# Optimization experiments

Hardware: AMD Instinct MI355X
Metric: run time of the kernel (lower is better)

## Reference

```python
import jax, jax.numpy as jnp
import numpy as np

H = 16       # query heads
KV = 4       # kv heads
BASE = 10000.0


def _rope(seq_len, head_dim, dtype):
    inv_freq = 1.0 / (BASE ** (jnp.arange(0, head_dim, 2, dtype=jnp.float32) / head_dim))
    t = jnp.arange(seq_len, dtype=jnp.float32)
    freqs = jnp.einsum('i,j->ij', t, inv_freq)          # [S, D/2]
    emb = jnp.concatenate([freqs, freqs], axis=-1)      # [S, D]
    return jnp.cos(emb).astype(dtype), jnp.sin(emb).astype(dtype)


def _rotate_half(x):
    x1, x2 = jnp.split(x, 2, axis=-1)
    return jnp.concatenate([-x2, x1], axis=-1)


def setup_inputs() -> dict:
    key = jax.random.key(0)
    ks = jax.random.split(key, 5)
    B, S, E = 2, 2048, 1024
    return {
        'x': jax.random.normal(ks[0], (B, S, E), jnp.float32),
        'wq': jax.random.normal(ks[1], (E, E), jnp.float32) * (E ** -0.5),
        'wk': jax.random.normal(ks[2], (KV * (E // H), E), jnp.float32) * (E ** -0.5),
        'wv': jax.random.normal(ks[3], (KV * (E // H), E), jnp.float32) * (E ** -0.5),
        'wo': jax.random.normal(ks[4], (E, E), jnp.float32) * (E ** -0.5),
    }


def reference(x, wq, wk, wv, wo):
    B, S, E = x.shape
    D = E // H
    G = H // KV  # query heads per kv head
    scale = D ** -0.5

    q = (x @ wq.T).reshape(B, S, H, D).transpose(0, 2, 1, 3)    # [B,H,S,D]
    k = (x @ wk.T).reshape(B, S, KV, D).transpose(0, 2, 1, 3)   # [B,KV,S,D]
    v = (x @ wv.T).reshape(B, S, KV, D).transpose(0, 2, 1, 3)   # [B,KV,S,D]

    cos, sin = _rope(S, D, x.dtype)                              # [S,D] each
    q = q * cos + _rotate_half(q) * sin
    k = k * cos + _rotate_half(k) * sin

    # GQA: group query heads per kv head instead of materializing repeated K/V
    qg = q.reshape(B, KV, G, S, D)
    scores = jnp.einsum('bkgsd,bktd->bkgst', qg, k) * scale      # [B,KV,G,S,S]
    causal = jnp.triu(jnp.ones((S, S), dtype=bool), k=1)
    scores = jnp.where(causal, jnp.finfo(scores.dtype).min, scores)
    attn = jax.nn.softmax(scores, axis=-1)
    out = jnp.einsum('bkgst,bktd->bkgsd', attn, v)               # [B,KV,G,S,D]
    out = out.reshape(B, H, S, D).transpose(0, 2, 1, 3).reshape(B, S, E)
    return out @ wo.T
```

## Files before the change

kernel.cpp:

```cpp
#include <hip/hip_runtime.h>
#include <stdint.h>

typedef unsigned short u16;
typedef __attribute__((ext_vector_type(8))) short s16x8;
typedef __attribute__((ext_vector_type(4))) float f32x4;
typedef __attribute__((ext_vector_type(4))) unsigned short u16x4;
typedef __attribute__((ext_vector_type(2))) unsigned int u32x2;


__device__ __forceinline__ u16 f2bf(float f) {
  unsigned u = __float_as_uint(f);
  unsigned r = (u + 0x7fffu + ((u >> 16) & 1u)) >> 16;
  return (u16)r;
}
__device__ __forceinline__ unsigned cvt_pk(float lo, float hi) {
  unsigned r;
  asm("v_cvt_pk_bf16_f32 %0, %1, %2" : "=v"(r) : "v"(lo), "v"(hi));
  return r;
}
__device__ __forceinline__ float exp2fast(float x) {
  return __builtin_amdgcn_exp2f(x);
}

typedef const __attribute__((address_space(1))) unsigned int* gas_ptr;
typedef __attribute__((address_space(3))) unsigned int* las_ptr;

__device__ __forceinline__ void g2l16(const void* g, void* l) {
  __builtin_amdgcn_global_load_lds((gas_ptr)g, (las_ptr)l, 16, 0, 0);
}

__device__ __forceinline__ void cvt4(const float* __restrict__ in, u16* __restrict__ out) {
  const f32x4 v = *(const f32x4*)in;
  u16x4 o;
  o[0] = f2bf(v[0]); o[1] = f2bf(v[1]); o[2] = f2bf(v[2]); o[3] = f2bf(v[3]);
  *(u16x4*)out = o;
}


__global__ void prep_kernel(const float* __restrict__ x,  const float* __restrict__ wq,
                            const float* __restrict__ wk, const float* __restrict__ wv,
                            const float* __restrict__ wo,
                            u16* __restrict__ xb, u16* __restrict__ wcat, u16* __restrict__ wob,
                            float* __restrict__ cosT, float* __restrict__ sinT) {
  const long id = (long)blockIdx.x * 256 + threadIdx.x;
  if (id < 262144) {
    cvt4(wq + id * 4, wcat + id * 4);
  } else if (id < 327680) {
    const long i = id - 262144;
    cvt4(wk + i * 4, wcat + 1048576 + i * 4);
  } else if (id < 393216) {
    const long i = id - 327680;
    cvt4(wv + i * 4, wcat + 1310720 + i * 4);
  } else if (id < 655360) {
    const long i = id - 393216;
    cvt4(wo + i * 4, wob + i * 4);
  } else if (id < 671744) {
    const long t = id - 655360;
#pragma unroll
    for (int u = 0; u < 4; ++u) {
      const long idx = t * 4 + u;
      const int s = (int)(idx >> 5), j = (int)(idx & 31);
      const double invd = exp(-(double)j * 0.2878231366242558);
      const float a = (float)s * (float)invd;
      cosT[idx] = cosf(a);
      sinT[idx] = sinf(a);
    }
  } else {
    const long i = id - 671744;
    cvt4(x + i * 4, xb + i * 4);
  }
}


__global__ __launch_bounds__(256, 2) void gemm_qkv_kernel(
    const u16* __restrict__ A, const u16* __restrict__ W,
    u16* __restrict__ qo, u16* __restrict__ ko, u16* __restrict__ vto,
    const float* __restrict__ cosT, const float* __restrict__ sinT) {
  const int K = 1024;
  __shared__ __align__(16) u16 As[2][128 * 64];
  __shared__ __align__(16) u16 Bs[2][128 * 64];
  const int tid = threadIdx.x;
  const int lane = tid & 63;
  const int wave = tid >> 6;
  const int g = lane >> 4, l15 = lane & 15;
  const int wr = wave >> 1, wc = wave & 1;
  const int bid = blockIdx.x;
  const int arowBlk = (bid & 7) * 4 + ((bid >> 3) & 3);
  const int wcolBlk = bid >> 5;
  const long arow0 = (long)arowBlk * 128;
  const long wrow0 = (long)wcolBlk * 128;
  const u16* Ab = A + arow0 * K;
  const u16* Wb = W + wrow0 * K;
  const bool isV = (wcolBlk >= 10);

  auto STAGE = [&](int buf, int k0) {
#pragma unroll
    for (int i = 0; i < 4; ++i) {
      const int lbase = i * 256 + wave * 64;
      const int c = lbase + lane;
      const int r = c >> 3, c8 = c & 7;
      const int cs = (c8 ^ (r & 7)) * 8;
      g2l16(Ab + (long)r * K + k0 + cs, (char*)As[buf] + lbase * 16);
      g2l16(Wb + (long)r * K + k0 + cs, (char*)Bs[buf] + lbase * 16);
    }
  };

  f32x4 acc[4][4] = {};
  int cur = 0;
  STAGE(0, 0);

  for (int k0 = 0; k0 < K; k0 += 64) {
    if (k0 + 64 < K) {
      STAGE(cur ^ 1, k0 + 64);
      asm volatile("s_waitcnt vmcnt(8)" ::: "memory");
    } else {
      asm volatile("s_waitcnt vmcnt(0)" ::: "memory");
    }
    __builtin_amdgcn_s_barrier();
#pragma unroll
    for (int ks = 0; ks < 2; ++ks) {
      s16x8 af[4], bfr[4];
#pragma unroll
      for (int m = 0; m < 4; ++m) {
        const int row = wr * 64 + m * 16 + l15;
        af[m] = *(const s16x8*)((const char*)As[cur] + row * 128 + (((ks * 4 + g) ^ (row & 7)) << 4));
      }
#pragma unroll
      for (int n = 0; n < 4; ++n) {
        const int row = wc * 64 + n * 16 + l15;
        bfr[n] = *(const s16x8*)((const char*)Bs[cur] + row * 128 + (((ks * 4 + g) ^ (row & 7)) << 4));
      }
      __builtin_amdgcn_s_setprio(1);
      if (!isV) {
#pragma unroll
        for (int m = 0; m < 4; ++m)
#pragma unroll
          for (int n = 0; n < 4; ++n)
            acc[m][n] = __builtin_amdgcn_mfma_f32_16x16x32_bf16(af[m], bfr[n], acc[m][n], 0, 0, 0);
      } else {
#pragma unroll
        for (int m = 0; m < 4; ++m)
#pragma unroll
          for (int n = 0; n < 4; ++n)
            acc[m][n] = __builtin_amdgcn_mfma_f32_16x16x32_bf16(bfr[m], af[n], acc[m][n], 0, 0, 0);
      }
      __builtin_amdgcn_s_setprio(0);
    }
    __builtin_amdgcn_s_barrier();
    cur ^= 1;
  }

  const int colBase = (int)wrow0 + wc * 64;
  const int j0 = l15;
  const float QSCALE = 0.18033688011112042f;

  if (colBase < 1024) {
    const int h2 = colBase >> 6;
#pragma unroll
    for (int m = 0; m < 4; ++m) {
      const int grow = (int)arow0 + wr * 64 + m * 16 + g * 4;
#pragma unroll
      for (int r = 0; r < 4; ++r) {
        const int row = grow + r;
        const int s = row & 2047, bb = row >> 11;
        const long ob = (((long)(bb * 16 + h2)) * 2048 + s) * 64;
        const float c0 = cosT[s * 32 + j0],      s0 = sinT[s * 32 + j0];
        const float c1 = cosT[s * 32 + 16 + j0], s1 = sinT[s * 32 + 16 + j0];
        qo[ob + j0]      = f2bf((acc[m][0][r] * c0 - acc[m][2][r] * s0) * QSCALE);
        qo[ob + 16 + j0] = f2bf((acc[m][1][r] * c1 - acc[m][3][r] * s1) * QSCALE);
        qo[ob + 32 + j0] = f2bf((acc[m][2][r] * c0 + acc[m][0][r] * s0) * QSCALE);
        qo[ob + 48 + j0] = f2bf((acc[m][3][r] * c1 + acc[m][1][r] * s1) * QSCALE);
      }
    }
  } else if (colBase < 1280) {
    const int kvh2 = (colBase - 1024) >> 6;
#pragma unroll
    for (int m = 0; m < 4; ++m) {
      const int grow = (int)arow0 + wr * 64 + m * 16 + g * 4;
#pragma unroll
      for (int r = 0; r < 4; ++r) {
        const int row = grow + r;
        const int s = row & 2047, bb = row >> 11;
        const long ob = (((long)(bb * 4 + kvh2)) * 2048 + s) * 64;
        const float c0 = cosT[s * 32 + j0],      s0 = sinT[s * 32 + j0];
        const float c1 = cosT[s * 32 + 16 + j0], s1 = sinT[s * 32 + 16 + j0];
        ko[ob + j0]      = f2bf(acc[m][0][r] * c0 - acc[m][2][r] * s0);
        ko[ob + 16 + j0] = f2bf(acc[m][1][r] * c1 - acc[m][3][r] * s1);
        ko[ob + 32 + j0] = f2bf(acc[m][2][r] * c0 + acc[m][0][r] * s0);
        ko[ob + 48 + j0] = f2bf(acc[m][3][r] * c1 + acc[m][1][r] * s1);
      }
    }
  } else {
    const int kvh2 = (colBase - 1280) >> 6;
    const int bb = (int)(arow0 >> 11);
    const int sBase = (int)(arow0 & 2047) + wr * 64;
    const long vrow0 = ((long)(bb * 4 + kvh2)) * 64;
#pragma unroll
    for (int mw = 0; mw < 4; ++mw) {
      const int d0 = mw * 16 + g * 4;
#pragma unroll
      for (int r = 0; r < 4; ++r) {
        const long db = (vrow0 + d0 + r) * 2048;
#pragma unroll
        for (int nx = 0; nx < 4; ++nx)
          vto[db + sBase + nx * 16 + l15] = f2bf(acc[mw][nx][r]);
      }
    }
  }
}


__global__ __launch_bounds__(256, 2) void gemm_out_kernel(
    const u16* __restrict__ A, const u16* __restrict__ W, float* __restrict__ Y) {
  const int K = 1024, N = 1024;
  __shared__ __align__(16) u16 As[2][128 * 64];
  __shared__ __align__(16) u16 Bs[2][128 * 64];
  const int tid = threadIdx.x;
  const int lane = tid & 63;
  const int wave = tid >> 6;
  const int g = lane >> 4, l15 = lane & 15;
  const int wr = wave >> 1, wc = wave & 1;
  const int bid = blockIdx.x;
  const int arowBlk = (bid & 7) * 4 + ((bid >> 3) & 3);
  const int wcolBlk = bid >> 5;
  const long arow0 = (long)arowBlk * 128;
  const long wrow0 = (long)wcolBlk * 128;
  const u16* Ab = A + arow0 * K;
  const u16* Wb = W + wrow0 * K;

  auto STAGE = [&](int buf, int k0) {
#pragma unroll
    for (int i = 0; i < 4; ++i) {
      const int lbase = i * 256 + wave * 64;
      const int c = lbase + lane;
      const int r = c >> 3, c8 = c & 7;
      const int cs = (c8 ^ (r & 7)) * 8;
      g2l16(Ab + (long)r * K + k0 + cs, (char*)As[buf] + lbase * 16);
      g2l16(Wb + (long)r * K + k0 + cs, (char*)Bs[buf] + lbase * 16);
    }
  };

  f32x4 acc[4][4] = {};
  int cur = 0;
  STAGE(0, 0);

  for (int k0 = 0; k0 < K; k0 += 64) {
    if (k0 + 64 < K) {
      STAGE(cur ^ 1, k0 + 64);
      asm volatile("s_waitcnt vmcnt(8)" ::: "memory");
    } else {
      asm volatile("s_waitcnt vmcnt(0)" ::: "memory");
    }
    __builtin_amdgcn_s_barrier();
#pragma unroll
    for (int ks = 0; ks < 2; ++ks) {
      s16x8 af[4], bfr[4];
#pragma unroll
      for (int m = 0; m < 4; ++m) {
        const int row = wr * 64 + m * 16 + l15;
        af[m] = *(const s16x8*)((const char*)As[cur] + row * 128 + (((ks * 4 + g) ^ (row & 7)) << 4));
      }
#pragma unroll
      for (int n = 0; n < 4; ++n) {
        const int row = wc * 64 + n * 16 + l15;
        bfr[n] = *(const s16x8*)((const char*)Bs[cur] + row * 128 + (((ks * 4 + g) ^ (row & 7)) << 4));
      }
      __builtin_amdgcn_s_setprio(1);
#pragma unroll
      for (int m = 0; m < 4; ++m)
#pragma unroll
        for (int n = 0; n < 4; ++n)
          acc[m][n] = __builtin_amdgcn_mfma_f32_16x16x32_bf16(af[m], bfr[n], acc[m][n], 0, 0, 0);
      __builtin_amdgcn_s_setprio(0);
    }
    __builtin_amdgcn_s_barrier();
    cur ^= 1;
  }

#pragma unroll
  for (int m = 0; m < 4; ++m)
#pragma unroll
    for (int n = 0; n < 4; ++n) {
      const long gr0 = arow0 + wr * 64 + m * 16 + g * 4;
      const long gc = wrow0 + wc * 64 + n * 16 + l15;
#pragma unroll
      for (int r = 0; r < 4; ++r)
        Y[(gr0 + r) * N + gc] = acc[m][n][r];
    }
}


__global__ __launch_bounds__(256, 3) void flash_kernel(
    const u16* __restrict__ qg,
    const u16* __restrict__ kg,
    const u16* __restrict__ vtg,
    u16* __restrict__ og) {
  const int tid = threadIdx.x, lane = tid & 63, w = tid >> 6;
  const int g = lane >> 4, l15 = lane & 15;

  const int bid = blockIdx.x;
  const int lid = (bid & 7) * 128 + (bid >> 3);
  const int qtIdx = lid & 31;
  const int h = (lid >> 5) & 15;
  const int b = lid >> 9;
  const int qt = (qtIdx & 1) ? (31 - (qtIdx >> 1)) : (qtIdx >> 1);
  const int kvh = h >> 2;

  __shared__ __align__(16) u16 Kl[2][64 * 64];
  __shared__ __align__(16) u16 Vl[2][64 * 64];
  __shared__ __align__(16) u16 Pl[4][16][72];

  const u16* Kp = kg  + ((long)(b * 4 + kvh)) * 2048 * 64;
  const u16* Vp = vtg + ((long)(b * 4 + kvh)) * 64 * 2048;

  auto STAGE = [&](int buf, int kt) {
#pragma unroll
    for (int j = 0; j < 2; ++j) {
      const int lbase = j * 256 + w * 64;
      const int c = lbase + lane;
      const int row = c >> 3, c8 = c & 7;
      const int cs = (c8 ^ (row & 7)) * 8;
      g2l16(Kp + ((long)(kt * 64 + row)) * 64 + cs, (char*)Kl[buf] + lbase * 16);
      g2l16(Vp + (long)row * 2048 + kt * 64 + cs,  (char*)Vl[buf] + lbase * 16);
    }
  };

  const u16* Qp = qg + (((long)(b * 16 + h)) * 2048 + qt * 64 + w * 16) * 64;
  const s16x8 qf0 = *(const s16x8*)(Qp + l15 * 64 + g * 8);
  const s16x8 qf1 = *(const s16x8*)(Qp + l15 * 64 + 32 + g * 8);

  f32x4 of[4] = {};
  float m = -1e30f, lsum = 0.f;
  const int qrow = qt * 64 + w * 16 + l15;

  int cur = 0;
  STAGE(0, 0);

#pragma unroll 1
  for (int kt = 0; kt <= qt; ++kt) {
    if (kt < qt) {
      STAGE(cur ^ 1, kt + 1);
      asm volatile("s_waitcnt vmcnt(4)" ::: "memory");
    } else {
      asm volatile("s_waitcnt vmcnt(0)" ::: "memory");
    }
    __builtin_amdgcn_s_barrier();
    const u16* Kb = Kl[cur];
    const u16* Vb = Vl[cur];

    f32x4 sf[4] = {};
    __builtin_amdgcn_s_setprio(1);
#pragma unroll
    for (int ks = 0; ks < 2; ++ks) {
      const s16x8 qv = ks ? qf1 : qf0;
#pragma unroll
      for (int fn = 0; fn < 4; ++fn) {
        const int row = fn * 16 + l15;
        const s16x8 kf = *(const s16x8*)((const char*)Kb + row * 128 + (((ks * 4 + g) ^ (row & 7)) << 4));
        sf[fn] = __builtin_amdgcn_mfma_f32_16x16x32_bf16(kf, qv, sf[fn], 0, 0, 0);
      }
    }
    __builtin_amdgcn_s_setprio(0);

    const bool diag = (kt == qt);
    float p[16];
#pragma unroll
    for (int fn = 0; fn < 4; ++fn)
#pragma unroll
      for (int r = 0; r < 4; ++r) {
        float sv = sf[fn][r];
        if (diag) {
          const int kv = kt * 64 + fn * 16 + 4 * g + r;
          if (kv > qrow) sv = -1e30f;
        }
        p[fn * 4 + r] = sv;
      }
    const float t0 = fmaxf(fmaxf(p[0], p[1]), p[2]);
    const float t1 = fmaxf(fmaxf(p[3], p[4]), p[5]);
    const float t2 = fmaxf(fmaxf(p[6], p[7]), p[8]);
    const float t3 = fmaxf(fmaxf(p[9], p[10]), p[11]);
    const float t4 = fmaxf(fmaxf(p[12], p[13]), p[14]);
    float mx = fmaxf(fmaxf(fmaxf(t0, t1), t2), fmaxf(fmaxf(t3, t4), p[15]));
    mx = fmaxf(mx, __shfl_xor(mx, 16));
    mx = fmaxf(mx, __shfl_xor(mx, 32));

    if (!__all(mx - m <= 11.0f)) {
      const float mn = fmaxf(m, mx);
      const float al = exp2fast(m - mn);
      m = mn;
      lsum *= al;
      float alq[4];
#pragma unroll
      for (int r = 0; r < 4; ++r) alq[r] = __shfl(al, 4 * g + r);
#pragma unroll
      for (int fd = 0; fd < 4; ++fd)
#pragma unroll
        for (int r = 0; r < 4; ++r) of[fd][r] *= alq[r];
    }

#pragma unroll
    for (int i = 0; i < 16; ++i) p[i] = exp2fast(p[i] - m);
    const float s0 = (p[0] + p[1]) + (p[2] + p[3]);
    const float s1 = (p[4] + p[5]) + (p[6] + p[7]);
    const float s2 = (p[8] + p[9]) + (p[10] + p[11]);
    const float s3 = (p[12] + p[13]) + (p[14] + p[15]);
    float rs = (s0 + s1) + (s2 + s3);
    rs += __shfl_xor(rs, 16);
    rs += __shfl_xor(rs, 32);
    lsum += rs;

    u16* Pw = &Pl[w][l15][0];
#pragma unroll
    for (int fn = 0; fn < 4; ++fn) {
      const u32x2 v2 = {cvt_pk(p[fn * 4 + 0], p[fn * 4 + 1]),
                        cvt_pk(p[fn * 4 + 2], p[fn * 4 + 3])};
      *(u32x2*)(Pw + fn * 16 + g * 4) = v2;
    }

    __builtin_amdgcn_s_setprio(1);
#pragma unroll
    for (int ks = 0; ks < 2; ++ks) {
      const s16x8 pa = *(const s16x8*)(&Pl[w][l15][ks * 32 + g * 8]);
#pragma unroll
      for (int fd = 0; fd < 4; ++fd) {
        const int vrow = fd * 16 + l15;
        const s16x8 vf = *(const s16x8*)((const char*)Vb + vrow * 128 + (((ks * 4 + g) ^ (vrow & 7)) << 4));
        of[fd] = __builtin_amdgcn_mfma_f32_16x16x32_bf16(pa, vf, of[fd], 0, 0, 0);
      }
    }
    __builtin_amdgcn_s_setprio(0);

    __builtin_amdgcn_s_barrier();
    cur ^= 1;
  }

  float linv[4];
#pragma unroll
  for (int r = 0; r < 4; ++r) linv[r] = 1.0f / __shfl(lsum, 4 * g + r);
  const long orow0 = (long)b * 2048 + qt * 64 + w * 16 + 4 * g;
#pragma unroll
  for (int r = 0; r < 4; ++r) {
    const long gb = (orow0 + r) * 1024 + h * 64;
#pragma unroll
    for (int fd = 0; fd < 4; ++fd)
      og[gb + fd * 16 + l15] = f2bf(of[fd][r] * linv[r]);
  }
}


extern "C" void kernel_launch(void* const* d_in, const int* in_sizes, int n_in,
                              void* d_out, int out_size, void* d_ws, size_t ws_size,
                              hipStream_t stream) {
  (void)in_sizes; (void)n_in; (void)out_size; (void)ws_size;
  const float* x  = (const float*)d_in[0];
  const float* wq = (const float*)d_in[1];
  const float* wk = (const float*)d_in[2];
  const float* wv = (const float*)d_in[3];
  const float* wo = (const float*)d_in[4];
  float* out = (float*)d_out;

  char* p = (char*)d_ws;
  auto alloc = [&](size_t bytes) { char* r = p; p += (bytes + 255) & ~(size_t)255; return r; };

  u16* xb    = (u16*)alloc(4096ull * 1024 * 2);
  u16* wcat  = (u16*)alloc(1536ull * 1024 * 2);
  u16* wob   = (u16*)alloc(1024ull * 1024 * 2);
  u16* qrb   = (u16*)alloc(4096ull * 1024 * 2);
  u16* krb   = (u16*)alloc(4096ull * 256 * 2);
  u16* vtb   = (u16*)alloc(4096ull * 256 * 2);
  u16* aob   = (u16*)alloc(4096ull * 1024 * 2);
  float* cosT = (float*)alloc(2048ull * 32 * 4);
  float* sinT = (float*)alloc(2048ull * 32 * 4);

  prep_kernel<<<6720, 256, 0, stream>>>(x, wq, wk, wv, wo, xb, wcat, wob, cosT, sinT);

  gemm_qkv_kernel<<<384, 256, 0, stream>>>(xb, wcat, qrb, krb, vtb, cosT, sinT);

  flash_kernel<<<1024, 256, 0, stream>>>(qrb, krb, vtb, aob);

  gemm_out_kernel<<<256, 256, 0, stream>>>(aob, wob, out);
}
```

Measured before the change: 194.0 us.

## Deepen GEMM pipelines to four stages and restructure flash attention tiling

Both GEMM kernels switch from a double-buffered K=64 pipeline to a four-deep K=32 pipeline with a new LDS swizzle. This keeps more global loads in flight and hides memory latency. The flash kernel now processes 128-key tiles, and each block handles a pair of query tiles (qt and 31-qt) in two passes, which balances the causal workload and halves the grid. The price is more LDS per flash block, occupancy reduced to 2, and extra P staging through LDS.

Measured after the change: 187.2 us. 1.04x faster.

```diff
diff --git a/kernel.cpp b/kernel.cpp
--- a/kernel.cpp
+++ b/kernel.cpp
@@ -77,8 +77,8 @@
     u16* __restrict__ qo, u16* __restrict__ ko, u16* __restrict__ vto,
     const float* __restrict__ cosT, const float* __restrict__ sinT) {
   const int K = 1024;
-  __shared__ __align__(16) u16 As[2][128 * 64];
-  __shared__ __align__(16) u16 Bs[2][128 * 64];
+  __shared__ __align__(16) u16 As[4][128 * 32];
+  __shared__ __align__(16) u16 Bs[4][128 * 32];
   const int tid = threadIdx.x;
   const int lane = tid & 63;
   const int wave = tid >> 6;
@@ -95,59 +95,61 @@
 
   auto STAGE = [&](int buf, int k0) {
 #pragma unroll
-    for (int i = 0; i < 4; ++i) {
-      const int lbase = i * 256 + wave * 64;
+    for (int j = 0; j < 2; ++j) {
+      const int lbase = j * 256 + wave * 64;
       const int c = lbase + lane;
-      const int r = c >> 3, c8 = c & 7;
-      const int cs = (c8 ^ (r & 7)) * 8;
+      const int r = c >> 2, c4 = c & 3;
+      const int cs = (c4 ^ ((r >> 1) & 3)) * 8;
       g2l16(Ab + (long)r * K + k0 + cs, (char*)As[buf] + lbase * 16);
       g2l16(Wb + (long)r * K + k0 + cs, (char*)Bs[buf] + lbase * 16);
     }
   };
 
   f32x4 acc[4][4] = {};
-  int cur = 0;
-  STAGE(0, 0);
-
-  for (int k0 = 0; k0 < K; k0 += 64) {
-    if (k0 + 64 < K) {
-      STAGE(cur ^ 1, k0 + 64);
+  STAGE(0, 0); STAGE(1, 32); STAGE(2, 64);
+
+#pragma unroll 1
+  for (int t = 0; t < 32; ++t) {
+    if (t < 29) {
+      STAGE((t + 3) & 3, (t + 3) * 32);
+      asm volatile("s_waitcnt vmcnt(12)" ::: "memory");
+    } else if (t == 29) {
       asm volatile("s_waitcnt vmcnt(8)" ::: "memory");
+    } else if (t == 30) {
+      asm volatile("s_waitcnt vmcnt(4)" ::: "memory");
     } else {
       asm volatile("s_waitcnt vmcnt(0)" ::: "memory");
     }
     __builtin_amdgcn_s_barrier();
-#pragma unroll
-    for (int ks = 0; ks < 2; ++ks) {
-      s16x8 af[4], bfr[4];
-#pragma unroll
-      for (int m = 0; m < 4; ++m) {
-        const int row = wr * 64 + m * 16 + l15;
-        af[m] = *(const s16x8*)((const char*)As[cur] + row * 128 + (((ks * 4 + g) ^ (row & 7)) << 4));
-      }
-#pragma unroll
-      for (int n = 0; n < 4; ++n) {
-        const int row = wc * 64 + n * 16 + l15;
-        bfr[n] = *(const s16x8*)((const char*)Bs[cur] + row * 128 + (((ks * 4 + g) ^ (row & 7)) << 4));
-      }
-      __builtin_amdgcn_s_setprio(1);
-      if (!isV) {
-#pragma unroll
-        for (int m = 0; m < 4; ++m)
-#pragma unroll
-          for (int n = 0; n < 4; ++n)
-            acc[m][n] = __builtin_amdgcn_mfma_f32_16x16x32_bf16(af[m], bfr[n], acc[m][n], 0, 0, 0);
-      } else {
-#pragma unroll
-        for (int m = 0; m < 4; ++m)
-#pragma unroll
-          for (int n = 0; n < 4; ++n)
-            acc[m][n] = __builtin_amdgcn_mfma_f32_16x16x32_bf16(bfr[m], af[n], acc[m][n], 0, 0, 0);
-      }
-      __builtin_amdgcn_s_setprio(0);
-    }
+    const u16* Ac = As[t & 3];
+    const u16* Bc = Bs[t & 3];
+    s16x8 af[4], bfr[4];
+#pragma unroll
+    for (int m = 0; m < 4; ++m) {
+      const int row = wr * 64 + m * 16 + l15;
+      af[m] = *(const s16x8*)((const char*)Ac + row * 64 + ((g ^ ((row >> 1) & 3)) << 4));
+    }
+#pragma unroll
+    for (int n = 0; n < 4; ++n) {
+      const int row = wc * 64 + n * 16 + l15;
+      bfr[n] = *(const s16x8*)((const char*)Bc + row * 64 + ((g ^ ((row >> 1) & 3)) << 4));
+    }
+    __builtin_amdgcn_s_setprio(1);
+    if (!isV) {
+#pragma unroll
+      for (int m = 0; m < 4; ++m)
+#pragma unroll
+        for (int n = 0; n < 4; ++n)
+          acc[m][n] = __builtin_amdgcn_mfma_f32_16x16x32_bf16(af[m], bfr[n], acc[m][n], 0, 0, 0);
+    } else {
+#pragma unroll
+      for (int m = 0; m < 4; ++m)
+#pragma unroll
+        for (int n = 0; n < 4; ++n)
+          acc[m][n] = __builtin_amdgcn_mfma_f32_16x16x32_bf16(bfr[m], af[n], acc[m][n], 0, 0, 0);
+    }
+    __builtin_amdgcn_s_setprio(0);
     __builtin_amdgcn_s_barrier();
-    cur ^= 1;
   }
 
   const int colBase = (int)wrow0 + wc * 64;
@@ -213,8 +215,8 @@
 __global__ __launch_bounds__(256, 2) void gemm_out_kernel(
     const u16* __restrict__ A, const u16* __restrict__ W, float* __restrict__ Y) {
   const int K = 1024, N = 1024;
-  __shared__ __align__(16) u16 As[2][128 * 64];
-  __shared__ __align__(16) u16 Bs[2][128 * 64];
+  __shared__ __align__(16) u16 As[4][128 * 32];
+  __shared__ __align__(16) u16 Bs[4][128 * 32];
   const int tid = threadIdx.x;
   const int lane = tid & 63;
   const int wave = tid >> 6;
@@ -230,51 +232,53 @@
 
   auto STAGE = [&](int buf, int k0) {
 #pragma unroll
-    for (int i = 0; i < 4; ++i) {
-      const int lbase = i * 256 + wave * 64;
+    for (int j = 0; j < 2; ++j) {
+      const int lbase = j * 256 + wave * 64;
       const int c = lbase + lane;
-      const int r = c >> 3, c8 = c & 7;
-      const int cs = (c8 ^ (r & 7)) * 8;
+      const int r = c >> 2, c4 = c & 3;
+      const int cs = (c4 ^ ((r >> 1) & 3)) * 8;
       g2l16(Ab + (long)r * K + k0 + cs, (char*)As[buf] + lbase * 16);
       g2l16(Wb + (long)r * K + k0 + cs, (char*)Bs[buf] + lbase * 16);
     }
   };
 
   f32x4 acc[4][4] = {};
-  int cur = 0;
-  STAGE(0, 0);
-
-  for (int k0 = 0; k0 < K; k0 += 64) {
-    if (k0 + 64 < K) {
-      STAGE(cur ^ 1, k0 + 64);
+  STAGE(0, 0); STAGE(1, 32); STAGE(2, 64);
+
+#pragma unroll 1
+  for (int t = 0; t < 32; ++t) {
+    if (t < 29) {
+      STAGE((t + 3) & 3, (t + 3) * 32);
+      asm volatile("s_waitcnt vmcnt(12)" ::: "memory");
+    } else if (t == 29) {
       asm volatile("s_waitcnt vmcnt(8)" ::: "memory");
+    } else if (t == 30) {
+      asm volatile("s_waitcnt vmcnt(4)" ::: "memory");
     } else {
       asm volatile("s_waitcnt vmcnt(0)" ::: "memory");
     }
     __builtin_amdgcn_s_barrier();
-#pragma unroll
-    for (int ks = 0; ks < 2; ++ks) {
-      s16x8 af[4], bfr[4];
-#pragma unroll
-      for (int m = 0; m < 4; ++m) {
-        const int row = wr * 64 + m * 16 + l15;
-        af[m] = *(const s16x8*)((const char*)As[cur] + row * 128 + (((ks * 4 + g) ^ (row & 7)) << 4));
-      }
-#pragma unroll
-      for (int n = 0; n < 4; ++n) {
-        const int row = wc * 64 + n * 16 + l15;
-        bfr[n] = *(const s16x8*)((const char*)Bs[cur] + row * 128 + (((ks * 4 + g) ^ (row & 7)) << 4));
-      }
-      __builtin_amdgcn_s_setprio(1);
-#pragma unroll
-      for (int m = 0; m < 4; ++m)
-#pragma unroll
-        for (int n = 0; n < 4; ++n)
-          acc[m][n] = __builtin_amdgcn_mfma_f32_16x16x32_bf16(af[m], bfr[n], acc[m][n], 0, 0, 0);
-      __builtin_amdgcn_s_setprio(0);
-    }
+    const u16* Ac = As[t & 3];
+    const u16* Bc = Bs[t & 3];
+    s16x8 af[4], bfr[4];
+#pragma unroll
+    for (int m = 0; m < 4; ++m) {
+      const int row = wr * 64 + m * 16 + l15;
+      af[m] = *(const s16x8*)((const char*)Ac + row * 64 + ((g ^ ((row >> 1) & 3)) << 4));
+    }
+#pragma unroll
+    for (int n = 0; n < 4; ++n) {
+      const int row = wc * 64 + n * 16 + l15;
+      bfr[n] = *(const s16x8*)((const char*)Bc + row * 64 + ((g ^ ((row >> 1) & 3)) << 4));
+    }
+    __builtin_amdgcn_s_setprio(1);
+#pragma unroll
+    for (int m = 0; m < 4; ++m)
+#pragma unroll
+      for (int n = 0; n < 4; ++n)
+        acc[m][n] = __builtin_amdgcn_mfma_f32_16x16x32_bf16(af[m], bfr[n], acc[m][n], 0, 0, 0);
+    __builtin_amdgcn_s_setprio(0);
     __builtin_amdgcn_s_barrier();
-    cur ^= 1;
   }
 
 #pragma unroll
@@ -290,7 +294,7 @@
 }
 
 
-__global__ __launch_bounds__(256, 3) void flash_kernel(
+__global__ __launch_bounds__(256, 2) void flash_kernel(
     const u16* __restrict__ qg,
     const u16* __restrict__ kg,
     const u16* __restrict__ vtg,
@@ -299,151 +303,180 @@
   const int g = lane >> 4, l15 = lane & 15;
 
   const int bid = blockIdx.x;
-  const int lid = (bid & 7) * 128 + (bid >> 3);
-  const int qtIdx = lid & 31;
-  const int h = (lid >> 5) & 15;
-  const int b = lid >> 9;
-  const int qt = (qtIdx & 1) ? (31 - (qtIdx >> 1)) : (qtIdx >> 1);
+  const int lid = (bid & 7) * 64 + (bid >> 3);
+  const int pr = lid & 15, h = (lid >> 4) & 15, b = lid >> 8;
   const int kvh = h >> 2;
 
-  __shared__ __align__(16) u16 Kl[2][64 * 64];
-  __shared__ __align__(16) u16 Vl[2][64 * 64];
-  __shared__ __align__(16) u16 Pl[4][16][72];
+  __shared__ __align__(16) u16 Kl[2][128 * 64];
+  __shared__ __align__(16) u16 Vl[2][64 * 128];
+  __shared__ __align__(16) u16 Pl[4][16][76];
 
   const u16* Kp = kg  + ((long)(b * 4 + kvh)) * 2048 * 64;
   const u16* Vp = vtg + ((long)(b * 4 + kvh)) * 64 * 2048;
 
-  auto STAGE = [&](int buf, int kt) {
-#pragma unroll
-    for (int j = 0; j < 2; ++j) {
+  auto STAGE = [&](int buf, int st) {
+#pragma unroll
+    for (int j = 0; j < 4; ++j) {
       const int lbase = j * 256 + w * 64;
       const int c = lbase + lane;
-      const int row = c >> 3, c8 = c & 7;
-      const int cs = (c8 ^ (row & 7)) * 8;
-      g2l16(Kp + ((long)(kt * 64 + row)) * 64 + cs, (char*)Kl[buf] + lbase * 16);
-      g2l16(Vp + (long)row * 2048 + kt * 64 + cs,  (char*)Vl[buf] + lbase * 16);
+      {
+        const int row = c >> 3, c8 = c & 7;
+        const int cs = (c8 ^ (row & 7)) * 8;
+        g2l16(Kp + ((long)(st * 128 + row)) * 64 + cs, (char*)Kl[buf] + lbase * 16);
+      }
+      {
+        const int row = c >> 4, c16 = c & 15;
+        const int cs = (c16 ^ (row & 7)) * 8;
+        g2l16(Vp + (long)row * 2048 + st * 128 + cs, (char*)Vl[buf] + lbase * 16);
+      }
     }
   };
 
-  const u16* Qp = qg + (((long)(b * 16 + h)) * 2048 + qt * 64 + w * 16) * 64;
-  const s16x8 qf0 = *(const s16x8*)(Qp + l15 * 64 + g * 8);
-  const s16x8 qf1 = *(const s16x8*)(Qp + l15 * 64 + 32 + g * 8);
-
-  f32x4 of[4] = {};
-  float m = -1e30f, lsum = 0.f;
-  const int qrow = qt * 64 + w * 16 + l15;
-
-  int cur = 0;
-  STAGE(0, 0);
-
 #pragma unroll 1
-  for (int kt = 0; kt <= qt; ++kt) {
-    if (kt < qt) {
-      STAGE(cur ^ 1, kt + 1);
-      asm volatile("s_waitcnt vmcnt(4)" ::: "memory");
-    } else {
-      asm volatile("s_waitcnt vmcnt(0)" ::: "memory");
-    }
-    __builtin_amdgcn_s_barrier();
-    const u16* Kb = Kl[cur];
-    const u16* Vb = Vl[cur];
-
-    f32x4 sf[4] = {};
-    __builtin_amdgcn_s_setprio(1);
-#pragma unroll
-    for (int ks = 0; ks < 2; ++ks) {
-      const s16x8 qv = ks ? qf1 : qf0;
+  for (int pass = 0; pass < 2; ++pass) {
+    const int qt = pass ? (31 - pr) : pr;
+    const int nst = (qt + 2) >> 1;
+    const u16* Qp = qg + (((long)(b * 16 + h)) * 2048 + qt * 64 + w * 16) * 64;
+    const s16x8 qf0 = *(const s16x8*)(Qp + l15 * 64 + g * 8);
+    const s16x8 qf1 = *(const s16x8*)(Qp + l15 * 64 + 32 + g * 8);
+
+    f32x4 of[4] = {};
+    float m = -1e30f, lsum = 0.f;
+    const int qrow = qt * 64 + w * 16 + l15;
+
+    int cur = 0;
+    STAGE(0, 0);
+
+#pragma unroll 1
+    for (int st = 0; st < nst; ++st) {
+      if (st + 1 < nst) {
+        STAGE(cur ^ 1, st + 1);
+        asm volatile("s_waitcnt vmcnt(8)" ::: "memory");
+      } else {
+        asm volatile("s_waitcnt vmcnt(0)" ::: "memory");
+      }
+      __builtin_amdgcn_s_barrier();
+      const u16* Kb = Kl[cur];
+      const u16* Vb = Vl[cur];
+
+      f32x4 sf[8] = {};
+      __builtin_amdgcn_s_setprio(1);
+#pragma unroll
+      for (int ks = 0; ks < 2; ++ks) {
+        const s16x8 qv = ks ? qf1 : qf0;
+#pragma unroll
+        for (int fn = 0; fn < 8; ++fn) {
+          const int row = fn * 16 + l15;
+          const s16x8 kf = *(const s16x8*)((const char*)Kb + row * 128 + (((ks * 4 + g) ^ (row & 7)) << 4));
+          sf[fn] = __builtin_amdgcn_mfma_f32_16x16x32_bf16(kf, qv, sf[fn], 0, 0, 0);
+        }
+      }
+      __builtin_amdgcn_s_setprio(0);
+
+      const bool diag = (st == nst - 1);
+      float p[32];
+#pragma unroll
+      for (int fn = 0; fn < 8; ++fn)
+#pragma unroll
+        for (int r = 0; r < 4; ++r) {
+          float sv = sf[fn][r];
+          if (diag) {
+            const int kv = st * 128 + fn * 16 + 4 * g + r;
+            if (kv > qrow) sv = -1e30f;
+          }
+          p[fn * 4 + r] = sv;
+        }
+
+      float t16[16];
+#pragma unroll
+      for (int i = 0; i < 16; ++i) t16[i] = fmaxf(p[i], p[i + 16]);
+#pragma unroll
+      for (int i = 0; i < 8; ++i) t16[i] = fmaxf(t16[i], t16[i + 8]);
+#pragma unroll
+      for (int i = 0; i < 4; ++i) t16[i] = fmaxf(t16[i], t16[i + 4]);
+      float mx = fmaxf(fmaxf(t16[0], t16[1]), fmaxf(t16[2], t16[3]));
+      mx = fmaxf(mx, __shfl_xor(mx, 16));
+      mx = fmaxf(mx, __shfl_xor(mx, 32));
+
+      if (!__all(mx - m <= 11.0f)) {
+        const float mn = fmaxf(m, mx);
+        const float al = exp2fast(m - mn);
+        m = mn;
+        lsum *= al;
+        float alq[4];
+#pragma unroll
+        for (int r = 0; r < 4; ++r) alq[r] = __shfl(al, 4 * g + r);
+#pragma unroll
+        for (int fd = 0; fd < 4; ++fd)
+#pragma unroll
+          for (int r = 0; r < 4; ++r) of[fd][r] *= alq[r];
+      }
+
+#pragma unroll
+      for (int i = 0; i < 32; ++i) p[i] = exp2fast(p[i] - m);
+      float s8[8];
+#pragma unroll
+      for (int i = 0; i < 8; ++i) s8[i] = (p[i * 4] + p[i * 4 + 1]) + (p[i * 4 + 2] + p[i * 4 + 3]);
+      float rs = ((s8[0] + s8[1]) + (s8[2] + s8[3])) + ((s8[4] + s8[5]) + (s8[6] + s8[7]));
+      rs += __shfl_xor(rs, 16);
+      rs += __shfl_xor(rs, 32);
+      lsum += rs;
+
+      u16* Pw = &Pl[w][l15][0];
+
 #pragma unroll
       for (int fn = 0; fn < 4; ++fn) {
-        const int row = fn * 16 + l15;
-        const s16x8 kf = *(const s16x8*)((const char*)Kb + row * 128 + (((ks * 4 + g) ^ (row & 7)) << 4));
-        sf[fn] = __builtin_amdgcn_mfma_f32_16x16x32_bf16(kf, qv, sf[fn], 0, 0, 0);
-      }
-    }
-    __builtin_amdgcn_s_setprio(0);
-
-    const bool diag = (kt == qt);
-    float p[16];
-#pragma unroll
-    for (int fn = 0; fn < 4; ++fn)
-#pragma unroll
-      for (int r = 0; r < 4; ++r) {
-        float sv = sf[fn][r];
-        if (diag) {
-          const int kv = kt * 64 + fn * 16 + 4 * g + r;
-          if (kv > qrow) sv = -1e30f;
+        const u32x2 v2 = {cvt_pk(p[fn * 4 + 0], p[fn * 4 + 1]),
+                          cvt_pk(p[fn * 4 + 2], p[fn * 4 + 3])};
+        *(u32x2*)(Pw + fn * 16 + g * 4) = v2;
+      }
+      __builtin_amdgcn_s_setprio(1);
+#pragma unroll
+      for (int ks = 0; ks < 2; ++ks) {
+        const s16x8 pa = *(const s16x8*)(Pw + ks * 32 + g * 8);
+#pragma unroll
+        for (int fd = 0; fd < 4; ++fd) {
+          const int vrow = fd * 16 + l15;
+          const s16x8 vf = *(const s16x8*)((const char*)Vb + vrow * 256 + (((ks * 4 + g) ^ (vrow & 7)) << 4));
+          of[fd] = __builtin_amdgcn_mfma_f32_16x16x32_bf16(pa, vf, of[fd], 0, 0, 0);
         }
-        p[fn * 4 + r] = sv;
-      }
-    const float t0 = fmaxf(fmaxf(p[0], p[1]), p[2]);
-    const float t1 = fmaxf(fmaxf(p[3], p[4]), p[5]);
-    const float t2 = fmaxf(fmaxf(p[6], p[7]), p[8]);
-    const float t3 = fmaxf(fmaxf(p[9], p[10]), p[11]);
-    const float t4 = fmaxf(fmaxf(p[12], p[13]), p[14]);
-    float mx = fmaxf(fmaxf(fmaxf(t0, t1), t2), fmaxf(fmaxf(t3, t4), p[15]));
-    mx = fmaxf(mx, __shfl_xor(mx, 16));
-    mx = fmaxf(mx, __shfl_xor(mx, 32));
-
-    if (!__all(mx - m <= 11.0f)) {
-      const float mn = fmaxf(m, mx);
-      const float al = exp2fast(m - mn);
-      m = mn;
-      lsum *= al;
-      float alq[4];
-#pragma unroll
-      for (int r = 0; r < 4; ++r) alq[r] = __shfl(al, 4 * g + r);
+      }
+      __builtin_amdgcn_s_setprio(0);
+
+#pragma unroll
+      for (int fn = 0; fn < 4; ++fn) {
+        const u32x2 v2 = {cvt_pk(p[16 + fn * 4 + 0], p[16 + fn * 4 + 1]),
+                          cvt_pk(p[16 + fn * 4 + 2], p[16 + fn * 4 + 3])};
+        *(u32x2*)(Pw + fn * 16 + g * 4) = v2;
+      }
+      __builtin_amdgcn_s_setprio(1);
+#pragma unroll
+      for (int ks = 2; ks < 4; ++ks) {
+        const s16x8 pa = *(const s16x8*)(Pw + (ks - 2) * 32 + g * 8);
+#pragma unroll
+        for (int fd = 0; fd < 4; ++fd) {
+          const int vrow = fd * 16 + l15;
+          const s16x8 vf = *(const s16x8*)((const char*)Vb + vrow * 256 + (((ks * 4 + g) ^ (vrow & 7)) << 4));
+          of[fd] = __builtin_amdgcn_mfma_f32_16x16x32_bf16(pa, vf, of[fd], 0, 0, 0);
+        }
+      }
+      __builtin_amdgcn_s_setprio(0);
+
+      __builtin_amdgcn_s_barrier();
+      cur ^= 1;
+    }
+
+    float linv[4];
+#pragma unroll
+    for (int r = 0; r < 4; ++r) linv[r] = 1.0f / __shfl(lsum, 4 * g + r);
+    const long orow0 = (long)b * 2048 + qt * 64 + w * 16 + 4 * g;
+#pragma unroll
+    for (int r = 0; r < 4; ++r) {
+      const long gb = (orow0 + r) * 1024 + h * 64;
 #pragma unroll
       for (int fd = 0; fd < 4; ++fd)
-#pragma unroll
-        for (int r = 0; r < 4; ++r) of[fd][r] *= alq[r];
-    }
-
-#pragma unroll
-    for (int i = 0; i < 16; ++i) p[i] = exp2fast(p[i] - m);
-    const float s0 = (p[0] + p[1]) + (p[2] + p[3]);
-    const float s1 = (p[4] + p[5]) + (p[6] + p[7]);
-    const float s2 = (p[8] + p[9]) + (p[10] + p[11]);
-    const float s3 = (p[12] + p[13]) + (p[14] + p[15]);
-    float rs = (s0 + s1) + (s2 + s3);
-    rs += __shfl_xor(rs, 16);
-    rs += __shfl_xor(rs, 32);
-    lsum += rs;
-
-    u16* Pw = &Pl[w][l15][0];
-#pragma unroll
-    for (int fn = 0; fn < 4; ++fn) {
-      const u32x2 v2 = {cvt_pk(p[fn * 4 + 0], p[fn * 4 + 1]),
-                        cvt_pk(p[fn * 4 + 2], p[fn * 4 + 3])};
-      *(u32x2*)(Pw + fn * 16 + g * 4) = v2;
-    }
-
-    __builtin_amdgcn_s_setprio(1);
-#pragma unroll
-    for (int ks = 0; ks < 2; ++ks) {
-      const s16x8 pa = *(const s16x8*)(&Pl[w][l15][ks * 32 + g * 8]);
-#pragma unroll
-      for (int fd = 0; fd < 4; ++fd) {
-        const int vrow = fd * 16 + l15;
-        const s16x8 vf = *(const s16x8*)((const char*)Vb + vrow * 128 + (((ks * 4 + g) ^ (vrow & 7)) << 4));
-        of[fd] = __builtin_amdgcn_mfma_f32_16x16x32_bf16(pa, vf, of[fd], 0, 0, 0);
-      }
-    }
-    __builtin_amdgcn_s_setprio(0);
-
-    __builtin_amdgcn_s_barrier();
-    cur ^= 1;
-  }
-
-  float linv[4];
-#pragma unroll
-  for (int r = 0; r < 4; ++r) linv[r] = 1.0f / __shfl(lsum, 4 * g + r);
-  const long orow0 = (long)b * 2048 + qt * 64 + w * 16 + 4 * g;
-#pragma unroll
-  for (int r = 0; r < 4; ++r) {
-    const long gb = (orow0 + r) * 1024 + h * 64;
-#pragma unroll
-    for (int fd = 0; fd < 4; ++fd)
-      og[gb + fd * 16 + l15] = f2bf(of[fd][r] * linv[r]);
+        og[gb + fd * 16 + l15] = f2bf(of[fd][r] * linv[r]);
+    }
   }
 }
 
@@ -476,7 +509,7 @@
 
   gemm_qkv_kernel<<<384, 256, 0, stream>>>(xb, wcat, qrb, krb, vtb, cosT, sinT);
 
-  flash_kernel<<<1024, 256, 0, stream>>>(qrb, krb, vtb, aob);
+  flash_kernel<<<512, 256, 0, stream>>>(qrb, krb, vtb, aob);
 
   gemm_out_kernel<<<256, 256, 0, stream>>>(aob, wob, out);
 }
```
